# Kernel tuning notes

Measured on AMD Instinct MI355X. Metric: run time of the kernel, lower is better.

## Reference

```python
import jax, jax.numpy as jnp
import numpy as np

EPS = 1e-5

def conv3x3(x, w, b):
    # x: [B,C,H,W], w: [O,I,3,3] -> SAME padding (pad=1)
    y = jax.lax.conv_general_dilated(x, w, (1, 1), 'SAME',
                                     dimension_numbers=('NCHW', 'OIHW', 'NCHW'))
    return y + b[None, :, None, None]

def batchnorm(x, g, b):
    # training-mode batch statistics over (B,H,W), biased variance (torch default)
    m = x.mean(axis=(0, 2, 3), keepdims=True)
    v = x.var(axis=(0, 2, 3), keepdims=True)
    return (x - m) / jnp.sqrt(v + EPS) * g[None, :, None, None] + b[None, :, None, None]

def setup_inputs() -> dict:
    key = jax.random.key(0)
    ks = jax.random.split(key, 24)
    B, Cin, Cout, T, H, W = 16, 256, 256, 256, 32, 32
    Cq = Cout // 8
    s = lambda fan: 1.0 / np.sqrt(fan)
    inp = {
        'x': jax.random.normal(ks[0], (B, Cin, H, W), jnp.float32),
        't': jax.random.normal(ks[1], (B, T), jnp.float32),
        # time_mlp: Linear(T,T) -> ReLU -> Linear(T,Cout)
        'w_t1': jax.random.normal(ks[2], (T, T), jnp.float32) * s(T),
        'b_t1': jax.random.normal(ks[3], (T,), jnp.float32) * s(T),
        'w_t2': jax.random.normal(ks[4], (Cout, T), jnp.float32) * s(T),
        'b_t2': jax.random.normal(ks[5], (Cout,), jnp.float32) * s(T),
        # convs (3x3, pad=1)
        'w_c1': jax.random.normal(ks[6], (Cout, Cin, 3, 3), jnp.float32) * s(Cin * 9),
        'b_c1': jax.random.normal(ks[7], (Cout,), jnp.float32) * s(Cin * 9),
        'w_c2': jax.random.normal(ks[8], (Cout, Cout, 3, 3), jnp.float32) * s(Cout * 9),
        'b_c2': jax.random.normal(ks[9], (Cout,), jnp.float32) * s(Cout * 9),
        'w_tr': jax.random.normal(ks[10], (Cout, Cout, 3, 3), jnp.float32) * s(Cout * 9),
        'b_tr': jax.random.normal(ks[11], (Cout,), jnp.float32) * s(Cout * 9),
        # batchnorm affine params
        'bn1_g': jnp.ones((Cout,), jnp.float32),
        'bn1_b': jnp.zeros((Cout,), jnp.float32),
        'bn2_g': jnp.ones((Cout,), jnp.float32),
        'bn2_b': jnp.zeros((Cout,), jnp.float32),
        # self-attention 1x1 convs (stored as [O,I])
        'wq': jax.random.normal(ks[12], (Cq, Cout), jnp.float32) * s(Cout),
        'bq': jax.random.normal(ks[13], (Cq,), jnp.float32) * s(Cout),
        'wk': jax.random.normal(ks[14], (Cq, Cout), jnp.float32) * s(Cout),
        'bk': jax.random.normal(ks[15], (Cq,), jnp.float32) * s(Cout),
        'wv': jax.random.normal(ks[16], (Cout, Cout), jnp.float32) * s(Cout),
        'bv': jax.random.normal(ks[17], (Cout,), jnp.float32) * s(Cout),
        # gamma is nn.Parameter(zeros(1)); use a random value so the residual branch is exercised
        'gamma': jax.random.normal(ks[18], (1,), jnp.float32),
    }
    return inp

def reference(x, t, w_t1, b_t1, w_t2, b_t2, w_c1, b_c1, w_c2, b_c2, w_tr, b_tr,
              bn1_g, bn1_b, bn2_g, bn2_b, wq, bq, wk, bk, wv, bv, gamma):
    # --- Block ---
    h = batchnorm(jax.nn.relu(conv3x3(x, w_c1, b_c1)), bn1_g, bn1_b)
    te = jax.nn.relu(t @ w_t1.T + b_t1)
    te = jax.nn.relu(te @ w_t2.T + b_t2)          # [B, Cout]
    h = h + te[:, :, None, None]
    h = batchnorm(jax.nn.relu(conv3x3(h, w_c2, b_c2)), bn2_g, bn2_b)
    y = conv3x3(h, w_tr, b_tr)                    # transform (up=False)
    # --- SelfAttention ---
    B, C, H, W = y.shape
    yf = y.reshape(B, C, H * W)                   # [B, C, N]
    Q = jnp.einsum('qc,bcn->bnq', wq, yf) + bq[None, None, :]   # [B, N, Cq]
    K = jnp.einsum('qc,bcn->bqn', wk, yf) + bk[None, :, None]   # [B, Cq, N]
    V = jnp.einsum('vc,bcn->bvn', wv, yf) + bv[None, :, None]   # [B, C, N]
    attn = jax.nn.softmax(jnp.einsum('bnq,bqm->bnm', Q, K), axis=-1)  # [B, N, N]
    out = jnp.einsum('bcm,bnm->bcn', V, attn).reshape(B, C, H, W)
    return gamma[0] * out + y
```

## Files before the change

### kernel.cpp

```cpp
#include <hip/hip_runtime.h>
#include <hip/hip_bf16.h>

using bf16 = __hip_bfloat16;

typedef __attribute__((ext_vector_type(8))) short bf16x8_t;
typedef __attribute__((ext_vector_type(4))) float f32x4_t;

__device__ __forceinline__ float b2f(bf16 x){ return __bfloat162float(x); }
__device__ __forceinline__ bf16  f2b(float x){ return __float2bfloat16(x); }
__device__ __forceinline__ unsigned short f2bu(float x){ bf16 h = __float2bfloat16(x); return *(unsigned short*)&h; }
__device__ __forceinline__ float bits2f(unsigned int lo16){ return __uint_as_float(lo16 << 16); }

__device__ __forceinline__ void gload16(const void* g, void* l) {
    __builtin_amdgcn_global_load_lds(
        (const __attribute__((address_space(1))) unsigned int*)g,
        (__attribute__((address_space(3))) unsigned int*)l, 16, 0, 0);
}


__global__ __launch_bounds__(256) void prep_all_k(
    const float* __restrict__ x, bf16* __restrict__ Xp0, bf16* __restrict__ Xp1,
    float* __restrict__ sums,
    const float* __restrict__ t, const float* __restrict__ w_t1, const float* __restrict__ b_t1,
    const float* __restrict__ w_t2, const float* __restrict__ b_t2, float* __restrict__ te,
    const float* __restrict__ w1, const float* __restrict__ w2, const float* __restrict__ w3,
    bf16* __restrict__ W1, bf16* __restrict__ W2, bf16* __restrict__ W3o,
    const float* __restrict__ wq, const float* __restrict__ wk, const float* __restrict__ wv,
    bf16* __restrict__ WQK, bf16* __restrict__ WVb)
{
    __shared__ char smem[64 * 65 * 4];
    const int blk = blockIdx.x;
    const int tid = threadIdx.x;

    if (blk < 1024) {
        float (*xs)[65] = (float(*)[65])smem;
        if (blk == 0) {
            sums[tid] = 0.f; sums[tid + 256] = 0.f; sums[tid + 512] = 0.f; sums[tid + 768] = 0.f;
        }
        const int b = blk >> 6, ct = (blk >> 4) & 3, nt = blk & 15;
        const int c0 = ct << 6, n0 = nt << 6;
        {
            const int cl = tid >> 2, nc = (tid & 3) << 4;
            const float* src = x + (size_t)((b << 8) + c0 + cl) * 1024 + n0 + nc;
            #pragma unroll
            for (int j = 0; j < 16; j += 4) {
                const float4 v = *(const float4*)(src + j);
                xs[cl][nc + j] = v.x; xs[cl][nc + j + 1] = v.y;
                xs[cl][nc + j + 2] = v.z; xs[cl][nc + j + 3] = v.w;
            }
        }
        __syncthreads();
        {
            const int nl = tid >> 2, cc = (tid & 3) << 4;
            const int n = n0 + nl;
            const int p = ((n >> 5) + 1) * 34 + (n & 31) + 1;
            unsigned int u[8];
            #pragma unroll
            for (int k = 0; k < 8; ++k)
                u[k] = (unsigned int)f2bu(xs[cc + 2 * k][nl]) | ((unsigned int)f2bu(xs[cc + 2 * k + 1][nl]) << 16);
            bf16* dst = Xp0 + (size_t)(b * 1156 + p) * 256 + c0 + cc;
            *(uint4*)dst = make_uint4(u[0], u[1], u[2], u[3]);
            *(uint4*)(dst + 8) = make_uint4(u[4], u[5], u[6], u[7]);
        }
    } else if (blk < 1792) {
        float* ls = (float*)smem;
        const int id = blk - 1024;
        const int co = id & 255;
        const int sel = id >> 8;
        const float* w = (sel == 0) ? w1 : (sel == 1) ? w2 : w3;
        bf16* dst = (sel == 0) ? W1 : (sel == 1) ? W2 : W3o;
        const float* src = w + (size_t)co * 2304;
        #pragma unroll
        for (int i = 0; i < 9; ++i) ls[tid + (i << 8)] = src[tid + (i << 8)];
        __syncthreads();
        #pragma unroll
        for (int off = 0; off < 9; ++off)
            dst[(size_t)(co * 9 + off) * 256 + tid] = f2b(ls[tid * 9 + off]);
    } else if (blk < 2112) {
        const int r = blk - 1792;
        if (r < 32)       WQK[r * 256 + tid] = f2b(wq[r * 256 + tid]);
        else if (r < 64)  WQK[r * 256 + tid] = f2b(wk[(r - 32) * 256 + tid]);
        else              WVb[(r - 64) * 256 + tid] = f2b(wv[(r - 64) * 256 + tid]);
    } else if (blk < 2128) {
        float* tr = (float*)smem;
        float* hid = tr + 256;
        const int b = blk - 2112, j = tid;
        tr[j] = t[(b << 8) + j];
        __syncthreads();
        float s = b_t1[j];
        const float* wp = w_t1 + j * 256;
        for (int k = 0; k < 256; ++k) s += tr[k] * wp[k];
        hid[j] = fmaxf(s, 0.f);
        __syncthreads();
        float s2 = b_t2[j];
        const float* wp2 = w_t2 + j * 256;
        for (int k = 0; k < 256; ++k) s2 += hid[k] * wp2[k];
        te[(b << 8) + j] = fmaxf(s2, 0.f);
    } else {
        const int idx = (blk - 2128) * 256 + tid;
        const int v = idx >> 6;
        const int o = (idx & 63) << 1;
        if (v < 4224) {
            const int buf = v / 2112;
            const int rem = v - buf * 2112;
            const int b = rem / 132;
            const int h = rem - b * 132;
            int p;
            if (h < 34)        p = h;
            else if (h < 68)   p = 1122 + (h - 34);
            else if (h < 100)  p = (h - 68 + 1) * 34;
            else               p = (h - 100 + 1) * 34 + 33;
            unsigned int* dst = (unsigned int*)((buf ? Xp1 : Xp0) + (size_t)(b * 1156 + p) * 256);
            dst[o] = 0u; dst[o + 1] = 0u;
        }
    }
}

template<bool RELU, bool STATS>
__global__ __launch_bounds__(512, 1) void conv_mfma_k(
    const bf16* __restrict__ Xp, const bf16* __restrict__ W3,
    const float* __restrict__ bias, bf16* __restrict__ outp, float* __restrict__ sums)
{
    __shared__ bf16 Als[2][16384];
    __shared__ bf16 Bls[3][8192];
    __shared__ float sstat[256];
    const int tid = threadIdx.x;
    const int wid = tid >> 6, lane = tid & 63;
    const int wm = wid >> 2, wn = wid & 3;
    const int blk = blockIdx.x;
    const int xc = blk & 7, tt = blk >> 3;
    const int b = xc + ((tt >> 4) << 3);
    const int tile = tt & 15, mt = tile >> 1, nt = tile & 1;
    const int m0 = mt << 7, co0 = nt << 7;

    if (STATS && tid < 256) sstat[tid] = 0.f;

    const bf16* xsl = Xp + (size_t)(b * 1156 + mt * 136) * 256;

    const int lrow = tid >> 3;
    const int sL8 = (((tid & 7) ^ (lrow & 7)) << 3);
    const bf16* bgp[2];
    #pragma unroll
    for (int i = 0; i < 2; ++i)
        bgp[i] = W3 + (size_t)(co0 + (i << 6) + lrow) * 2304 + sL8;

    const int apix = (wid << 3) + (lane >> 3);
    const int aj0 = lane & 7;

    const int rsel = lane & 15, lg = lane >> 4;
    const int s0 = ((lg ^ (lane & 7)) << 3);
    const int s1 = (((lg + 4) ^ (lane & 7)) << 3);
    const int bbase = ((wn << 5) + rsel) << 6;
    int dbase[4];
    #pragma unroll
    for (int mi = 0; mi < 4; ++mi)
        dbase[mi] = ((wm << 1) + (mi >> 1)) * 34 + ((mi & 1) << 4) + rsel;

    f32x4_t acc[4][2];
    #pragma unroll
    for (int mi = 0; mi < 4; ++mi)
        #pragma unroll
        for (int ni = 0; ni < 2; ++ni)
            acc[mi][ni] = (f32x4_t){0.f, 0.f, 0.f, 0.f};

    auto STAGE_A = [&](int cic, int buf) {
        #pragma unroll
        for (int i = 0; i < 4; ++i) {
            const int pix = (i << 6) + apix;
            const int j = aj0 ^ (pix & 7);
            gload16(xsl + (size_t)pix * 256 + (cic << 6) + (j << 3),
                    &Als[buf][((i << 9) + (wid << 6)) << 3]);
        }
    };
    auto STAGE_B = [&](int st, int buf) {
        const int koff = ((st % 9) << 8) + ((st / 9) << 6);
        #pragma unroll
        for (int i = 0; i < 2; ++i)
            gload16(bgp[i] + koff, &Bls[buf][((i << 6) + (wid << 3)) << 6]);
    };

    STAGE_A(0, 0);
    STAGE_B(0, 0);
    STAGE_B(1, 1);

    #pragma unroll
    for (int st = 0; st < 36; ++st) {
        if (st == 35)         asm volatile("s_waitcnt vmcnt(0)" ::: "memory");
        else if (st % 9 == 8) asm volatile("s_waitcnt vmcnt(6)" ::: "memory");
        else                  asm volatile("s_waitcnt vmcnt(2)" ::: "memory");
        __builtin_amdgcn_s_barrier();
        asm volatile("" ::: "memory");
        const int cic = st / 9, off = st % 9;
        const int doff = (off / 3) * 34 + (off % 3);
        const bf16* abuf = Als[cic & 1];
        const bf16* bbuf = Bls[st % 3];
        #pragma unroll
        for (int kh = 0; kh < 2; ++kh) {
            const int sk = kh ? s1 : s0;
            bf16x8_t av[4], bv[2];
            #pragma unroll
            for (int mi = 0; mi < 4; ++mi) {
                const int sp = dbase[mi] + doff;
                av[mi] = *(const bf16x8_t*)((const char*)abuf +
                            (sp << 7) + ((((kh << 2) + lg) ^ (sp & 7)) << 4));
            }
            #pragma unroll
            for (int ni = 0; ni < 2; ++ni)
                bv[ni] = *(const bf16x8_t*)(bbuf + bbase + (ni << 10) + sk);
            #pragma unroll
            for (int mi = 0; mi < 4; ++mi)
                #pragma unroll
                for (int ni = 0; ni < 2; ++ni)
                    acc[mi][ni] = __builtin_amdgcn_mfma_f32_16x16x32_bf16(
                        av[mi], bv[ni], acc[mi][ni], 0, 0, 0);
        }
        if (st + 2 < 36) STAGE_B(st + 2, (st + 2) % 3);
        if (off == 7 && st < 27) STAGE_A(cic + 1, (cic + 1) & 1);
    }

    const int cr = lg << 2;
    const int cc = rsel;
    #pragma unroll
    for (int ni = 0; ni < 2; ++ni) {
        const int co = co0 + (wn << 5) + (ni << 4) + cc;
        const float bb = bias[co];
        float ssum = 0.f, ssq = 0.f;
        #pragma unroll
        for (int mi = 0; mi < 4; ++mi) {
            const int n = m0 + (wm << 6) + (mi << 4) + cr;
            #pragma unroll
            for (int j = 0; j < 4; ++j) {
                float v = acc[mi][ni][j] + bb;
                if (RELU) v = fmaxf(v, 0.f);
                outp[(size_t)((b << 10) + n + j) * 256 + co] = f2b(v);
                if (STATS) { ssum += v; ssq += v * v; }
            }
        }
        if (STATS) {
            ssum += __shfl_xor(ssum, 16); ssum += __shfl_xor(ssum, 32);
            ssq  += __shfl_xor(ssq, 16);  ssq  += __shfl_xor(ssq, 32);
            if (lane < 16) {
                const int ch = (wn << 5) + (ni << 4) + cc;
                atomicAdd(&sstat[ch * 2], ssum);
                atomicAdd(&sstat[ch * 2 + 1], ssq);
            }
        }
    }
    if (STATS) {
        __syncthreads();
        if (tid < 128) {
            atomicAdd(&sums[co0 + tid], sstat[tid * 2]);
            atomicAdd(&sums[256 + co0 + tid], sstat[tid * 2 + 1]);
        }
    }
}

template<bool TE>
__global__ __launch_bounds__(256) void bn_apply_T_k(
    const bf16* __restrict__ a, const float* __restrict__ sums,
    const float* __restrict__ g, const float* __restrict__ bb,
    const float* __restrict__ te, bf16* __restrict__ Xp)
{
    const int t = threadIdx.x;
    const int row = blockIdx.x * 8 + (t >> 5);
    const int c0 = (t & 31) << 3;
    const int b = row >> 10, n = row & 1023;
    const uint4 u = *(const uint4*)(a + (size_t)row * 256 + c0);
    const unsigned int w[4] = {u.x, u.y, u.z, u.w};
    float scv[8], shv[8];
    #pragma unroll
    for (int k = 0; k < 8; ++k) {
        const int c = c0 + k;
        const float m = sums[c] * (1.f / 16384.f);
        const float var = sums[256 + c] * (1.f / 16384.f) - m * m;
        const float sc = g[c] * rsqrtf(var + 1e-5f);
        scv[k] = sc;
        shv[k] = bb[c] - m * sc + (TE ? te[(b << 8) + c] : 0.f);
    }
    unsigned int o[4];
    #pragma unroll
    for (int k = 0; k < 4; ++k) {
        const float v0 = bits2f(w[k] & 0xffffu) * scv[2*k] + shv[2*k];
        const float v1 = __uint_as_float(w[k] & 0xffff0000u) * scv[2*k+1] + shv[2*k+1];
        o[k] = (unsigned int)f2bu(v0) | ((unsigned int)f2bu(v1) << 16);
    }
    const int p = ((n >> 5) + 1) * 34 + (n & 31) + 1;
    *(uint4*)(Xp + (size_t)(b * 1156 + p) * 256 + c0) = make_uint4(o[0], o[1], o[2], o[3]);
}

__global__ __launch_bounds__(512, 1) void qkv_mfma_k(
    const bf16* __restrict__ WVb, const bf16* __restrict__ Yt,
    const float* __restrict__ bvp, bf16* __restrict__ Vb,
    const bf16* __restrict__ WQK, const float* __restrict__ bq,
    const float* __restrict__ bk, bf16* __restrict__ QKb)
{
    __shared__ bf16 Als[3][128 * 64];
    __shared__ bf16 Bls[3][128 * 64];
    const int tid = threadIdx.x;
    const int wid = tid >> 6, lane = tid & 63;

    if (blockIdx.x >= 256) {
        const int blk2 = blockIdx.x - 256;
        const int b = blk2 >> 3, m0 = (blk2 & 7) << 7;
        const int n0w = m0 + (wid << 4);
        const bf16* arow = Yt + (size_t)((b << 10) + n0w + (lane & 15)) * 256 + ((lane >> 4) << 3);
        const int boff = ((lane >> 4) << 3);
        f32x4_t acc[4];
        #pragma unroll
        for (int ni = 0; ni < 4; ++ni) acc[ni] = (f32x4_t){0.f,0.f,0.f,0.f};
        for (int k0 = 0; k0 < 256; k0 += 32) {
            const bf16x8_t av = *(const bf16x8_t*)(arow + k0);
            #pragma unroll
            for (int ni = 0; ni < 4; ++ni) {
                const bf16x8_t bv = *(const bf16x8_t*)(WQK + (ni * 16 + (lane & 15)) * 256 + k0 + boff);
                acc[ni] = __builtin_amdgcn_mfma_f32_16x16x32_bf16(av, bv, acc[ni], 0, 0, 0);
            }
        }
        const int cr = (lane >> 4) << 2, cc = lane & 15;
        #pragma unroll
        for (int ni = 0; ni < 4; ++ni) {
            const int q = ni * 16 + cc;
            const float bias = (q < 32) ? bq[q] : bk[q - 32];
            #pragma unroll
            for (int j = 0; j < 4; ++j) {
                const int n = n0w + cr + j;
                QKb[(size_t)((b << 10) + n) * 64 + q] = f2b(acc[ni][j] + bias);
            }
        }
        return;
    }

    const int wm = wid >> 2, wn = wid & 3;
    const int blk = blockIdx.x;
    const int xc = blk & 7, tt = blk >> 3;
    const int b = xc + ((tt >> 4) << 3);
    const int tile = tt & 15, vt = tile >> 3, nt = tile & 7;
    const int v0 = vt << 7, n0 = nt << 7;

    const int lrow = tid >> 3;
    const int sL8 = (((tid & 7) ^ (lrow & 7)) << 3);
    const bf16* agp[2]; const bf16* bgp[2];
    #pragma unroll
    for (int i = 0; i < 2; ++i) {
        const int r = (i << 6) + lrow;
        agp[i] = WVb + (size_t)(v0 + r) * 256 + sL8;
        bgp[i] = Yt + (size_t)((b << 10) + n0 + r) * 256 + sL8;
    }
    const int rsel = lane & 15;
    const int s0 = (((lane >> 4) ^ (lane & 7)) << 3);
    const int s1 = ((((lane >> 4) + 4) ^ (lane & 7)) << 3);
    const int abase = ((wm << 6) + rsel) << 6;
    const int bbase = ((wn << 5) + rsel) << 6;

    f32x4_t acc[4][2];
    #pragma unroll
    for (int mi = 0; mi < 4; ++mi)
        #pragma unroll
        for (int ni = 0; ni < 2; ++ni)
            acc[mi][ni] = (f32x4_t){0.f,0.f,0.f,0.f};

    auto STAGE = [&](int kt2, int buf) {
        const int koff = kt2 << 6;
        #pragma unroll
        for (int i = 0; i < 2; ++i) {
            gload16(agp[i] + koff, &Als[buf][((i << 6) + (wid << 3)) << 6]);
            gload16(bgp[i] + koff, &Bls[buf][((i << 6) + (wid << 3)) << 6]);
        }
    };

    STAGE(0, 0); STAGE(1, 1);
    for (int kt = 0; kt < 4; ++kt) {
        if (kt < 3) asm volatile("s_waitcnt vmcnt(4)" ::: "memory");
        else        asm volatile("s_waitcnt vmcnt(0)" ::: "memory");
        __builtin_amdgcn_s_barrier();
        asm volatile("" ::: "memory");
        const int cur = kt % 3;
        #pragma unroll
        for (int kh = 0; kh < 2; ++kh) {
            const int sk = kh ? s1 : s0;
            bf16x8_t av[4], bv[2];
            #pragma unroll
            for (int mi = 0; mi < 4; ++mi)
                av[mi] = *(const bf16x8_t*)(&Als[cur][abase + (mi << 10) + sk]);
            #pragma unroll
            for (int ni = 0; ni < 2; ++ni)
                bv[ni] = *(const bf16x8_t*)(&Bls[cur][bbase + (ni << 10) + sk]);
            #pragma unroll
            for (int mi = 0; mi < 4; ++mi)
                #pragma unroll
                for (int ni = 0; ni < 2; ++ni)
                    acc[mi][ni] = __builtin_amdgcn_mfma_f32_16x16x32_bf16(
                        av[mi], bv[ni], acc[mi][ni], 0, 0, 0);
        }
        if (kt + 2 < 4) STAGE(kt + 2, (kt + 2) % 3);
    }

    const int cr = (lane >> 4) << 2, cc = lane & 15;
    #pragma unroll
    for (int mi = 0; mi < 4; ++mi) {
        #pragma unroll
        for (int j = 0; j < 4; ++j) {
            const int v = v0 + (wm << 6) + (mi << 4) + cr + j;
            const float bb = bvp[v];
            #pragma unroll
            for (int ni = 0; ni < 2; ++ni) {
                const int n = n0 + (wn << 5) + (ni << 4) + cc;
                Vb[(size_t)((b << 8) + v) * 1024 + n] = f2b(acc[mi][ni][j] + bb);
            }
        }
    }
}

__global__ __launch_bounds__(256) void softmax_k(
    const bf16* __restrict__ QKb, bf16* __restrict__ P, float* __restrict__ invs)
{
    const int b = blockIdx.x >> 5, n0 = (blockIdx.x & 31) << 5;
    const int tid = threadIdx.x, wid = tid >> 6, lane = tid & 63;
    const int m0w = wid << 8;
    __shared__ float wred[4][32];

    const bf16* qbase = QKb + (size_t)((b << 10) + n0) * 64;
    const int koff = (lane >> 4) << 3;
    bf16x8_t qf[2];
    #pragma unroll
    for (int nt = 0; nt < 2; ++nt)
        qf[nt] = *(const bf16x8_t*)(qbase + (nt * 16 + (lane & 15)) * 64 + koff);
    const bf16* kbase = QKb + (size_t)(b << 10) * 64 + 32;

    float mx[2] = {-3.0e38f, -3.0e38f};
    for (int mi = 0; mi < 16; ++mi) {
        const bf16x8_t kf = *(const bf16x8_t*)(kbase + (m0w + mi * 16 + (lane & 15)) * 64 + koff);
        #pragma unroll
        for (int nt = 0; nt < 2; ++nt) {
            f32x4_t s = (f32x4_t){0.f,0.f,0.f,0.f};
            s = __builtin_amdgcn_mfma_f32_16x16x32_bf16(kf, qf[nt], s, 0, 0, 0);
            mx[nt] = fmaxf(mx[nt], fmaxf(fmaxf(s[0], s[1]), fmaxf(s[2], s[3])));
        }
    }
    #pragma unroll
    for (int nt = 0; nt < 2; ++nt) {
        mx[nt] = fmaxf(mx[nt], __shfl_xor(mx[nt], 16));
        mx[nt] = fmaxf(mx[nt], __shfl_xor(mx[nt], 32));
        if (lane < 16) wred[wid][nt * 16 + lane] = mx[nt];
    }
    __syncthreads();
    float rm[2];
    #pragma unroll
    for (int nt = 0; nt < 2; ++nt) {
        const int c = nt * 16 + (lane & 15);
        rm[nt] = fmaxf(fmaxf(wred[0][c], wred[1][c]), fmaxf(wred[2][c], wred[3][c]));
    }
    __syncthreads();

    float sm[2] = {0.f, 0.f};
    for (int mi = 0; mi < 16; ++mi) {
        const bf16x8_t kf = *(const bf16x8_t*)(kbase + (m0w + mi * 16 + (lane & 15)) * 64 + koff);
        #pragma unroll
        for (int nt = 0; nt < 2; ++nt) {
            f32x4_t s = (f32x4_t){0.f,0.f,0.f,0.f};
            s = __builtin_amdgcn_mfma_f32_16x16x32_bf16(kf, qf[nt], s, 0, 0, 0);
            const float p0 = __expf(s[0] - rm[nt]);
            const float p1 = __expf(s[1] - rm[nt]);
            const float p2 = __expf(s[2] - rm[nt]);
            const float p3 = __expf(s[3] - rm[nt]);
            sm[nt] += (p0 + p1) + (p2 + p3);
            uint2 u;
            u.x = (unsigned int)f2bu(p0) | ((unsigned int)f2bu(p1) << 16);
            u.y = (unsigned int)f2bu(p2) | ((unsigned int)f2bu(p3) << 16);
            const int n = n0 + nt * 16 + (lane & 15);
            const int m = m0w + mi * 16 + ((lane >> 4) << 2);
            *(uint2*)(P + (size_t)((b << 10) + n) * 1024 + m) = u;
        }
    }
    #pragma unroll
    for (int nt = 0; nt < 2; ++nt) {
        sm[nt] += __shfl_xor(sm[nt], 16);
        sm[nt] += __shfl_xor(sm[nt], 32);
        if (lane < 16) wred[wid][nt * 16 + lane] = sm[nt];
    }
    __syncthreads();
    if (tid < 32) {
        const float total = wred[0][tid] + wred[1][tid] + wred[2][tid] + wred[3][tid];
        invs[(b << 10) + n0 + tid] = 1.f / total;
    }
}

__global__ __launch_bounds__(512, 1) void pv_mfma_k(
    const bf16* __restrict__ Vb, const bf16* __restrict__ P,
    const float* __restrict__ invs, const bf16* __restrict__ Yt,
    const float* __restrict__ gamma, float* __restrict__ out)
{
    __shared__ bf16 Als[3][128 * 64];
    __shared__ bf16 Bls[3][128 * 64];
    const int tid = threadIdx.x;
    const int wid = tid >> 6, lane = tid & 63;
    const int wm = wid >> 2, wn = wid & 3;
    const int blk = blockIdx.x;
    const int xc = blk & 7, tt = blk >> 3;
    const int b = xc + ((tt >> 4) << 3);
    const int tile = tt & 15, ct = tile >> 3, nt = tile & 7;
    const int c0 = ct << 7, n0 = nt << 7;

    const int lrow = tid >> 3;
    const int sL8 = (((tid & 7) ^ (lrow & 7)) << 3);
    const bf16* agp[2]; const bf16* bgp[2];
    #pragma unroll
    for (int i = 0; i < 2; ++i) {
        const int r = (i << 6) + lrow;
        agp[i] = Vb + (size_t)((b << 8) + c0 + r) * 1024 + sL8;
        bgp[i] = P + (size_t)((b << 10) + n0 + r) * 1024 + sL8;
    }
    const int rsel = lane & 15;
    const int s0 = (((lane >> 4) ^ (lane & 7)) << 3);
    const int s1 = ((((lane >> 4) + 4) ^ (lane & 7)) << 3);
    const int abase = ((wm << 6) + rsel) << 6;
    const int bbase = ((wn << 5) + rsel) << 6;

    f32x4_t acc[4][2];
    #pragma unroll
    for (int mi = 0; mi < 4; ++mi)
        #pragma unroll
        for (int ni = 0; ni < 2; ++ni)
            acc[mi][ni] = (f32x4_t){0.f,0.f,0.f,0.f};

    auto STAGE = [&](int kt2, int buf) {
        const int koff = kt2 << 6;
        #pragma unroll
        for (int i = 0; i < 2; ++i) {
            gload16(agp[i] + koff, &Als[buf][((i << 6) + (wid << 3)) << 6]);
            gload16(bgp[i] + koff, &Bls[buf][((i << 6) + (wid << 3)) << 6]);
        }
    };

    STAGE(0, 0); STAGE(1, 1);
    for (int kt = 0; kt < 16; ++kt) {
        if (kt < 15) asm volatile("s_waitcnt vmcnt(4)" ::: "memory");
        else         asm volatile("s_waitcnt vmcnt(0)" ::: "memory");
        __builtin_amdgcn_s_barrier();
        asm volatile("" ::: "memory");
        const int cur = kt % 3;
        #pragma unroll
        for (int kh = 0; kh < 2; ++kh) {
            const int sk = kh ? s1 : s0;
            bf16x8_t av[4], bv[2];
            #pragma unroll
            for (int mi = 0; mi < 4; ++mi)
                av[mi] = *(const bf16x8_t*)(&Als[cur][abase + (mi << 10) + sk]);
            #pragma unroll
            for (int ni = 0; ni < 2; ++ni)
                bv[ni] = *(const bf16x8_t*)(&Bls[cur][bbase + (ni << 10) + sk]);
            #pragma unroll
            for (int mi = 0; mi < 4; ++mi)
                #pragma unroll
                for (int ni = 0; ni < 2; ++ni)
                    acc[mi][ni] = __builtin_amdgcn_mfma_f32_16x16x32_bf16(
                        av[mi], bv[ni], acc[mi][ni], 0, 0, 0);
        }
        if (kt + 2 < 16) STAGE(kt + 2, (kt + 2) % 3);
    }

    const float g = gamma[0];
    const int cr = (lane >> 4) << 2, cc = lane & 15;
    #pragma unroll
    for (int ni = 0; ni < 2; ++ni) {
        const int n = n0 + (wn << 5) + (ni << 4) + cc;
        const float gi = g * invs[(b << 10) + n];
        #pragma unroll
        for (int mi = 0; mi < 4; ++mi) {
            const int c = c0 + (wm << 6) + (mi << 4) + cr;
            const bf16* yp = Yt + (size_t)((b << 10) + n) * 256 + c;
            #pragma unroll
            for (int j = 0; j < 4; ++j)
                out[(size_t)((b << 8) + c + j) * 1024 + n] = gi * acc[mi][ni][j] + b2f(yp[j]);
        }
    }
}

extern "C" void kernel_launch(void* const* d_in, const int* in_sizes, int n_in,
                              void* d_out, int out_size, void* d_ws, size_t ws_size,
                              hipStream_t stream)
{
    const float* x     = (const float*)d_in[0];
    const float* t     = (const float*)d_in[1];
    const float* w_t1  = (const float*)d_in[2];
    const float* b_t1  = (const float*)d_in[3];
    const float* w_t2  = (const float*)d_in[4];
    const float* b_t2  = (const float*)d_in[5];
    const float* w_c1  = (const float*)d_in[6];
    const float* b_c1  = (const float*)d_in[7];
    const float* w_c2  = (const float*)d_in[8];
    const float* b_c2  = (const float*)d_in[9];
    const float* w_tr  = (const float*)d_in[10];
    const float* b_tr  = (const float*)d_in[11];
    const float* bn1g  = (const float*)d_in[12];
    const float* bn1b  = (const float*)d_in[13];
    const float* bn2g  = (const float*)d_in[14];
    const float* bn2b  = (const float*)d_in[15];
    const float* wq    = (const float*)d_in[16];
    const float* bq    = (const float*)d_in[17];
    const float* wk    = (const float*)d_in[18];
    const float* bk    = (const float*)d_in[19];
    const float* wv    = (const float*)d_in[20];
    const float* bv    = (const float*)d_in[21];
    const float* gamma = (const float*)d_in[22];
    float* out = (float*)d_out;

    char* ws = (char*)d_ws;
    float* te    = (float*)(ws + 0);
    float* sums1 = (float*)(ws + 16384);
    float* sums2 = (float*)(ws + 18432);
    char* base = ws + 32768;
    bf16* W3_1 = (bf16*)(base);
    bf16* W3_2 = (bf16*)(base + 1179648);
    bf16* W3_3 = (bf16*)(base + 2359296);
    bf16* Xp0  = (bf16*)(base + 3538944);
    bf16* Xp1  = (bf16*)(base + 13008896);
    bf16* Craw = (bf16*)(base + 22478848);
    bf16* P    = (bf16*)(base);
    bf16* Yt   = (bf16*)(base + 33554432);
    bf16* QKb  = (bf16*)(base + 41943040);
    bf16* Vb   = (bf16*)(base + 44040192);
    float* invs= (float*)(base + 52428800);
    bf16* WQK  = (bf16*)(base + 52494336);
    bf16* WVb  = (bf16*)(base + 52527104);

    prep_all_k<<<3184, 256, 0, stream>>>(
        x, Xp0, Xp1, sums1,
        t, w_t1, b_t1, w_t2, b_t2, te,
        w_c1, w_c2, w_tr, W3_1, W3_2, W3_3,
        wq, wk, wv, WQK, WVb);

    conv_mfma_k<true, true><<<256, 512, 0, stream>>>(Xp0, W3_1, b_c1, Craw, sums1);
    bn_apply_T_k<true><<<2048, 256, 0, stream>>>(Craw, sums1, bn1g, bn1b, te, Xp1);

    conv_mfma_k<true, true><<<256, 512, 0, stream>>>(Xp1, W3_2, b_c2, Craw, sums2);
    bn_apply_T_k<false><<<2048, 256, 0, stream>>>(Craw, sums2, bn2g, bn2b, nullptr, Xp0);

    conv_mfma_k<false, false><<<256, 512, 0, stream>>>(Xp0, W3_3, b_tr, Yt, nullptr);

    qkv_mfma_k<<<384, 512, 0, stream>>>(WVb, Yt, bv, Vb, WQK, bq, bk, QKb);
    softmax_k<<<512, 256, 0, stream>>>(QKb, P, invs);
    pv_mfma_k<<<256, 512, 0, stream>>>(Vb, P, invs, Yt, gamma, out);
}
```

Measured before the change: 149.5 us.

## Fuse conv/BN chain into one cooperative kernel with grid syncs

Replaces the five separate launches (three convs, two BN-apply passes) with one cooperative persistent kernel of 256 blocks that runs each phase in turn, separated by grid.sync(). The BN phase now has each block handle 64 rows with the scale and shift computed once, and loads the time embedding as float4. The aim is to remove launch overhead and inter-kernel gaps. In exchange, the BN phase runs on only 256 blocks instead of 2048, and the grid barriers add their own cost.

```diff
diff --git a/kernel.cpp b/kernel.cpp
--- a/kernel.cpp
+++ b/kernel.cpp
@@ -1,5 +1,8 @@
 #include <hip/hip_runtime.h>
 #include <hip/hip_bf16.h>
+#include <hip/hip_cooperative_groups.h>
+
+namespace cg = cooperative_groups;
 
 using bf16 = __hip_bfloat16;
 
@@ -117,23 +120,20 @@
 }
 
 template<bool RELU, bool STATS>
-__global__ __launch_bounds__(512, 1) void conv_mfma_k(
+__device__ __forceinline__ void conv_phase(
     const bf16* __restrict__ Xp, const bf16* __restrict__ W3,
-    const float* __restrict__ bias, bf16* __restrict__ outp, float* __restrict__ sums)
-{
-    __shared__ bf16 Als[2][16384];
-    __shared__ bf16 Bls[3][8192];
-    __shared__ float sstat[256];
-    const int tid = threadIdx.x;
+    const float* __restrict__ bias, bf16* __restrict__ outp, float* __restrict__ sums,
+    bf16* Als, bf16* Bls, float* sstat, const int blk, const int tid)
+{
     const int wid = tid >> 6, lane = tid & 63;
     const int wm = wid >> 2, wn = wid & 3;
-    const int blk = blockIdx.x;
     const int xc = blk & 7, tt = blk >> 3;
     const int b = xc + ((tt >> 4) << 3);
     const int tile = tt & 15, mt = tile >> 1, nt = tile & 1;
     const int m0 = mt << 7, co0 = nt << 7;
 
     if (STATS && tid < 256) sstat[tid] = 0.f;
+    if (STATS) __syncthreads();
 
     const bf16* xsl = Xp + (size_t)(b * 1156 + mt * 136) * 256;
 
@@ -169,14 +169,14 @@
             const int pix = (i << 6) + apix;
             const int j = aj0 ^ (pix & 7);
             gload16(xsl + (size_t)pix * 256 + (cic << 6) + (j << 3),
-                    &Als[buf][((i << 9) + (wid << 6)) << 3]);
+                    &Als[(buf << 14) + (((i << 9) + (wid << 6)) << 3)]);
         }
     };
     auto STAGE_B = [&](int st, int buf) {
         const int koff = ((st % 9) << 8) + ((st / 9) << 6);
         #pragma unroll
         for (int i = 0; i < 2; ++i)
-            gload16(bgp[i] + koff, &Bls[buf][((i << 6) + (wid << 3)) << 6]);
+            gload16(bgp[i] + koff, &Bls[(buf << 13) + (((i << 6) + (wid << 3)) << 6)]);
     };
 
     STAGE_A(0, 0);
@@ -192,8 +192,8 @@
         asm volatile("" ::: "memory");
         const int cic = st / 9, off = st % 9;
         const int doff = (off / 3) * 34 + (off % 3);
-        const bf16* abuf = Als[cic & 1];
-        const bf16* bbuf = Bls[st % 3];
+        const bf16* abuf = Als + ((cic & 1) << 14);
+        const bf16* bbuf = Bls + ((st % 3) << 13);
         #pragma unroll
         for (int kh = 0; kh < 2; ++kh) {
             const int sk = kh ? s1 : s0;
@@ -256,17 +256,13 @@
 }
 
 template<bool TE>
-__global__ __launch_bounds__(256) void bn_apply_T_k(
+__device__ __forceinline__ void bn_phase(
     const bf16* __restrict__ a, const float* __restrict__ sums,
     const float* __restrict__ g, const float* __restrict__ bb,
-    const float* __restrict__ te, bf16* __restrict__ Xp)
-{
-    const int t = threadIdx.x;
-    const int row = blockIdx.x * 8 + (t >> 5);
-    const int c0 = (t & 31) << 3;
-    const int b = row >> 10, n = row & 1023;
-    const uint4 u = *(const uint4*)(a + (size_t)row * 256 + c0);
-    const unsigned int w[4] = {u.x, u.y, u.z, u.w};
+    const float* __restrict__ te, bf16* __restrict__ Xp,
+    const int blk, const int tid)
+{
+    const int c0 = (tid & 31) << 3;
     float scv[8], shv[8];
     #pragma unroll
     for (int k = 0; k < 8; ++k) {
@@ -275,17 +271,60 @@
         const float var = sums[256 + c] * (1.f / 16384.f) - m * m;
         const float sc = g[c] * rsqrtf(var + 1e-5f);
         scv[k] = sc;
-        shv[k] = bb[c] - m * sc + (TE ? te[(b << 8) + c] : 0.f);
-    }
-    unsigned int o[4];
-    #pragma unroll
-    for (int k = 0; k < 4; ++k) {
-        const float v0 = bits2f(w[k] & 0xffffu) * scv[2*k] + shv[2*k];
-        const float v1 = __uint_as_float(w[k] & 0xffff0000u) * scv[2*k+1] + shv[2*k+1];
-        o[k] = (unsigned int)f2bu(v0) | ((unsigned int)f2bu(v1) << 16);
-    }
-    const int p = ((n >> 5) + 1) * 34 + (n & 31) + 1;
-    *(uint4*)(Xp + (size_t)(b * 1156 + p) * 256 + c0) = make_uint4(o[0], o[1], o[2], o[3]);
+        shv[k] = bb[c] - m * sc;
+    }
+    #pragma unroll
+    for (int it = 0; it < 4; ++it) {
+        const int row = blk * 64 + it * 16 + (tid >> 5);
+        const int b = row >> 10, n = row & 1023;
+        const uint4 u = *(const uint4*)(a + (size_t)row * 256 + c0);
+        const unsigned int w[4] = {u.x, u.y, u.z, u.w};
+        float tev[8] = {0,0,0,0,0,0,0,0};
+        if (TE) {
+            const float4 t0 = *(const float4*)(te + (b << 8) + c0);
+            const float4 t1 = *(const float4*)(te + (b << 8) + c0 + 4);
+            tev[0]=t0.x; tev[1]=t0.y; tev[2]=t0.z; tev[3]=t0.w;
+            tev[4]=t1.x; tev[5]=t1.y; tev[6]=t1.z; tev[7]=t1.w;
+        }
+        unsigned int o[4];
+        #pragma unroll
+        for (int k = 0; k < 4; ++k) {
+            const float v0 = bits2f(w[k] & 0xffffu) * scv[2*k] + shv[2*k] + tev[2*k];
+            const float v1 = __uint_as_float(w[k] & 0xffff0000u) * scv[2*k+1] + shv[2*k+1] + tev[2*k+1];
+            o[k] = (unsigned int)f2bu(v0) | ((unsigned int)f2bu(v1) << 16);
+        }
+        const int p = ((n >> 5) + 1) * 34 + (n & 31) + 1;
+        *(uint4*)(Xp + (size_t)(b * 1156 + p) * 256 + c0) = make_uint4(o[0], o[1], o[2], o[3]);
+    }
+}
+
+__global__ __launch_bounds__(512, 1) void conv_chain_k(
+    bf16* Xp0, bf16* Xp1, bf16* Craw, bf16* Yt,
+    const bf16* W1, const bf16* W2, const bf16* W3,
+    const float* b1, const float* b2, const float* b3,
+    float* sums1, float* sums2,
+    const float* bn1g, const float* bn1b, const float* bn2g, const float* bn2b,
+    const float* te)
+{
+    __shared__ bf16 Als[2 * 16384];
+    __shared__ bf16 Bls[3 * 8192];
+    __shared__ float sstat[256];
+    cg::grid_group grid = cg::this_grid();
+    const int blk = blockIdx.x, tid = threadIdx.x;
+
+    conv_phase<true, true>(Xp0, W1, b1, Craw, sums1, Als, Bls, sstat, blk, tid);
+    __threadfence();
+    grid.sync();
+    bn_phase<true>(Craw, sums1, bn1g, bn1b, te, Xp1, blk, tid);
+    __threadfence();
+    grid.sync();
+    conv_phase<true, true>(Xp1, W2, b2, Craw, sums2, Als, Bls, sstat, blk, tid);
+    __threadfence();
+    grid.sync();
+    bn_phase<false>(Craw, sums2, bn2g, bn2b, nullptr, Xp0, blk, tid);
+    __threadfence();
+    grid.sync();
+    conv_phase<false, false>(Xp0, W3, b3, Yt, nullptr, Als, Bls, sstat, blk, tid);
 }
 
 __global__ __launch_bounds__(512, 1) void qkv_mfma_k(
@@ -630,13 +669,18 @@
         w_c1, w_c2, w_tr, W3_1, W3_2, W3_3,
         wq, wk, wv, WQK, WVb);
 
-    conv_mfma_k<true, true><<<256, 512, 0, stream>>>(Xp0, W3_1, b_c1, Craw, sums1);
-    bn_apply_T_k<true><<<2048, 256, 0, stream>>>(Craw, sums1, bn1g, bn1b, te, Xp1);
-
-    conv_mfma_k<true, true><<<256, 512, 0, stream>>>(Xp1, W3_2, b_c2, Craw, sums2);
-    bn_apply_T_k<false><<<2048, 256, 0, stream>>>(Craw, sums2, bn2g, bn2b, nullptr, Xp0);
-
-    conv_mfma_k<false, false><<<256, 512, 0, stream>>>(Xp0, W3_3, b_tr, Yt, nullptr);
+    {
+        void* args[] = {
+            (void*)&Xp0, (void*)&Xp1, (void*)&Craw, (void*)&Yt,
+            (void*)&W3_1, (void*)&W3_2, (void*)&W3_3,
+            (void*)&b_c1, (void*)&b_c2, (void*)&b_tr,
+            (void*)&sums1, (void*)&sums2,
+            (void*)&bn1g, (void*)&bn1b, (void*)&bn2g, (void*)&bn2b,
+            (void*)&te
+        };
+        hipLaunchCooperativeKernel((void*)conv_chain_k, dim3(256), dim3(512),
+                                   args, 0, stream);
+    }
 
     qkv_mfma_k<<<384, 512, 0, stream>>>(WVb, Yt, bv, Vb, WQK, bq, bk, QKb);
     softmax_k<<<512, 256, 0, stream>>>(QKb, P, invs);
```

New measurement: 470.8 us. 3.15x slower.
